# Kernel optimization log

Hardware: AMD Instinct MI355X
Metric: run time of the kernel (lower is better)

The kernel has to match this reference:

```python
import jax, jax.numpy as jnp
import numpy as np

NUM_HEADS = 12
DIM_HEADS = 8  # number of sub-heads the depth is split into


def _split_into_heads(x, num_heads, dim_heads):
    # x: [B, S, E] -> [B, H, D, S, sub]  (D = dim_heads, sub = E/(H*D))
    B, S, E = x.shape
    depth = E // num_heads
    sub = depth // dim_heads
    x = x.reshape(B, S, num_heads, dim_heads, sub)
    return x.transpose(0, 2, 3, 1, 4)  # [B, H, D, S, sub]


def setup_inputs() -> dict:
    key = jax.random.key(0)
    ks = jax.random.split(key, 8)
    B, S, E = 2, 1024, 768
    sc_in = 1.0 / np.sqrt(E)
    return {
        "k": jax.random.normal(ks[0], (B, S, E), dtype=jnp.float32),
        "q": jax.random.normal(ks[1], (B, S, E), dtype=jnp.float32),
        "Wq_w": jax.random.normal(ks[2], (E, E), dtype=jnp.float32) * sc_in,
        "Wq_b": jax.random.normal(ks[3], (E,), dtype=jnp.float32) * 0.01,
        "Wk_w": jax.random.normal(ks[4], (E, E), dtype=jnp.float32) * sc_in,
        "Wk_b": jax.random.normal(ks[5], (E,), dtype=jnp.float32) * 0.01,
        "lin_w": jax.random.normal(ks[6], (DIM_HEADS,), dtype=jnp.float32) * (1.0 / np.sqrt(DIM_HEADS)),
        "lin_b": jax.random.normal(ks[7], (), dtype=jnp.float32) * 0.01,
    }


def reference(k, q, Wq_w, Wq_b, Wk_w, Wk_b, lin_w, lin_b):
    # Linear projections (torch Linear: x @ W^T + b)
    qp = q @ Wq_w.T + Wq_b  # [B, S, E]
    kp = k @ Wk_w.T + Wk_b  # [B, S, E]

    qh = _split_into_heads(qp, NUM_HEADS, DIM_HEADS)  # [B, H, D, S, sub]
    kh = _split_into_heads(kp, NUM_HEADS, DIM_HEADS)  # [B, H, D, S, sub]
    sub = kh.shape[-1]
    scale = 1.0 / np.sqrt(sub).astype(np.float32)

    # Original: scores[b,h,d,i,j] = (qh @ kh^T)/sqrt(sub), permute to [b,h,i,j,d],
    # dropout (identity at eval), then Linear(D,1).squeeze(-1).
    out = jnp.einsum("bhdis,bhdjs,d->bhij", qh, kh, lin_w) * scale + lin_b
    return out  # [B, H, S, S]
```

## Files before the change

kernel.cpp:

```cpp
#include <hip/hip_runtime.h>
#include <hip/hip_bf16.h>

#define S_ 1024
#define E_ 768
#define H_ 12

typedef __bf16  bf16x8 __attribute__((ext_vector_type(8)));
typedef float   f32x4  __attribute__((ext_vector_type(4)));
typedef unsigned short u16x8 __attribute__((ext_vector_type(8)));
typedef unsigned short u16x4 __attribute__((ext_vector_type(4)));

__device__ __forceinline__ unsigned short f2bf(float f) {
    union { float f; unsigned u; } a; a.f = f;
    unsigned u = a.u;
    u += 0x7FFFu + ((u >> 16) & 1u);
    return (unsigned short)(u >> 16);
}

__device__ __forceinline__ u16x8 pack8(float4 a, float4 b) {
    u16x8 o;
    o[0] = f2bf(a.x); o[1] = f2bf(a.y); o[2] = f2bf(a.z); o[3] = f2bf(a.w);
    o[4] = f2bf(b.x); o[5] = f2bf(b.y); o[6] = f2bf(b.z); o[7] = f2bf(b.w);
    return o;
}

__device__ __forceinline__ bf16x8 ld_frag(const char* lbase, int row, int kk, int lane) {
    int cbyte = (kk * 64 + ((lane >> 4) * 16)) ^ ((row & 7) << 4);
    return *(const bf16x8*)(lbase + row * 128 + cbyte);
}

__global__ __launch_bounds__(256) void prep_w_kernel(
    const float* __restrict__ Wq, const float* __restrict__ bq,
    const float* __restrict__ Wk, const float* __restrict__ lin_w,
    unsigned short* __restrict__ Wqbf, unsigned short* __restrict__ Wkbf,
    float* __restrict__ bqs)
{
    const float invs = 0.35355339059327373f;
    int idx4 = blockIdx.x * 256 + threadIdx.x;
    int i = idx4 * 4;
    if (blockIdx.z == 0) {
        int n = i / E_;
        float w = lin_w[(n & 63) >> 3] * invs;
        float4 v = *(const float4*)(Wq + i);
        ushort4 o = make_ushort4(f2bf(v.x * w), f2bf(v.y * w), f2bf(v.z * w), f2bf(v.w * w));
        *(ushort4*)(Wqbf + i) = o;
        if (idx4 < E_) bqs[idx4] = bq[idx4] * (lin_w[(idx4 & 63) >> 3] * invs);
    } else {
        float4 v = *(const float4*)(Wk + i);
        ushort4 o = make_ushort4(f2bf(v.x), f2bf(v.y), f2bf(v.z), f2bf(v.w));
        *(ushort4*)(Wkbf + i) = o;
    }
}

__global__ __launch_bounds__(256) void proj_kernel(
    const float* __restrict__ q_in, const float* __restrict__ k_in,
    const unsigned short* __restrict__ Wqbf, const unsigned short* __restrict__ Wkbf,
    const float* __restrict__ bqs, const float* __restrict__ bk,
    unsigned short* __restrict__ qs, unsigned short* __restrict__ kp)
{
    __shared__ char lds[32768];

    int lid = blockIdx.x;
    int swz = (lid & 7) * 96 + (lid >> 3);
    int z  = swz / 384;
    int rem = swz - z * 384;
    int ty = rem / 12, tx = rem - ty * 12;
    int tm = ty * 64, tn = tx * 64;

    const float* X          = z ? k_in : q_in;
    const unsigned short* W = z ? Wkbf : Wqbf;
    const float* bias       = z ? bk   : bqs;
    unsigned short* P       = z ? kp   : qs;

    int tid = threadIdx.x, lane = tid & 63, wid = tid >> 6;
    int wn = wid >> 1, wm = wid & 1;

    int c0 = tid,        r0 = c0 >> 3, g0 = ((c0 & 7) ^ (r0 & 7)) * 8;
    int c1 = 256 + tid,  r1 = c1 >> 3, g1 = ((c1 & 7) ^ (r1 & 7)) * 8;

    const float* Xg          = X + (size_t)tm * E_;
    const unsigned short* Wg = W + (size_t)tn * E_;

    float4 xv0, xv1, xv2, xv3;
#define LOADX(kb) { \
    const float* xs0 = Xg + r0 * E_ + (kb) + g0; xv0 = *(const float4*)xs0; xv1 = *(const float4*)(xs0 + 4); \
    const float* xs1 = Xg + r1 * E_ + (kb) + g1; xv2 = *(const float4*)xs1; xv3 = *(const float4*)(xs1 + 4); }
#define WRITEX(buf) { \
    char* xb = lds + (buf) * 8192; \
    *(u16x8*)(xb + c0 * 16) = pack8(xv0, xv1); \
    *(u16x8*)(xb + c1 * 16) = pack8(xv2, xv3); }
#define STAGEW(kb, buf) { \
    char* wb = lds + 16384 + (buf) * 8192; \
    __builtin_amdgcn_global_load_lds( \
        (const __attribute__((address_space(1))) void*)(Wg + (size_t)r0 * E_ + (kb) + g0), \
        (__attribute__((address_space(3))) void*)(wb + c0 * 16), 16, 0, 0); \
    __builtin_amdgcn_global_load_lds( \
        (const __attribute__((address_space(1))) void*)(Wg + (size_t)r1 * E_ + (kb) + g1), \
        (__attribute__((address_space(3))) void*)(wb + c1 * 16), 16, 0, 0); }

    f32x4 acc[2][2];
#pragma unroll
    for (int nj = 0; nj < 2; ++nj) {
        int n0 = tn + wn * 32 + nj * 16 + ((lane >> 4) << 2);
        float4 b4 = *(const float4*)(bias + n0);
#pragma unroll
        for (int mi = 0; mi < 2; ++mi)
            acc[nj][mi] = f32x4{b4.x, b4.y, b4.z, b4.w};
    }

#define COMPSTEP(buf) { \
    const char* Xc = lds + (buf) * 8192; \
    const char* Wc = lds + 16384 + (buf) * 8192; \
    _Pragma("unroll") \
    for (int kk = 0; kk < 2; ++kk) { \
        bf16x8 a0 = ld_frag(Wc, wn * 32 + (lane & 15), kk, lane); \
        bf16x8 a1 = ld_frag(Wc, wn * 32 + 16 + (lane & 15), kk, lane); \
        bf16x8 b0 = ld_frag(Xc, wm * 32 + (lane & 15), kk, lane); \
        bf16x8 b1 = ld_frag(Xc, wm * 32 + 16 + (lane & 15), kk, lane); \
        acc[0][0] = __builtin_amdgcn_mfma_f32_16x16x32_bf16(a0, b0, acc[0][0], 0, 0, 0); \
        acc[0][1] = __builtin_amdgcn_mfma_f32_16x16x32_bf16(a0, b1, acc[0][1], 0, 0, 0); \
        acc[1][0] = __builtin_amdgcn_mfma_f32_16x16x32_bf16(a1, b0, acc[1][0], 0, 0, 0); \
        acc[1][1] = __builtin_amdgcn_mfma_f32_16x16x32_bf16(a1, b1, acc[1][1], 0, 0, 0); \
    } }

    STAGEW(0, 0);
    LOADX(0);
    WRITEX(0);
    __syncthreads();
    int cur = 0;
#pragma unroll 2
    for (int t = 0; t < 11; ++t) {
        STAGEW((t + 1) * 64, cur ^ 1);
        LOADX((t + 1) * 64);
        COMPSTEP(cur);
        WRITEX(cur ^ 1);
        __syncthreads();
        cur ^= 1;
    }
    COMPSTEP(cur);

#pragma unroll
    for (int nj = 0; nj < 2; ++nj)
#pragma unroll
        for (int mi = 0; mi < 2; ++mi) {
            int n0 = tn + wn * 32 + nj * 16 + ((lane >> 4) << 2);
            int m  = tm + wm * 32 + mi * 16 + (lane & 15);
            u16x4 pk;
            pk[0] = f2bf(acc[nj][mi][0]); pk[1] = f2bf(acc[nj][mi][1]);
            pk[2] = f2bf(acc[nj][mi][2]); pk[3] = f2bf(acc[nj][mi][3]);
            *(u16x4*)(P + (size_t)m * E_ + n0) = pk;
        }
#undef LOADX
#undef WRITEX
#undef STAGEW
#undef COMPSTEP
}

__global__ __launch_bounds__(256) void scores_kernel(
    const unsigned short* __restrict__ qs, const unsigned short* __restrict__ kp,
    const float* __restrict__ lin_b, float* __restrict__ out)
{
    __shared__ char lds[32768];

    int lid = blockIdx.x;
    int swz = (lid & 7) * 96 + (lid >> 3);
    int z   = swz >> 5;
    int rem = swz & 31;
    int iy  = rem >> 2, jx = rem & 3;
    int b = z / H_, h = z - b * H_;

    int tid = threadIdx.x, lane = tid & 63, wid = tid >> 6;
    int wj = wid >> 1, wi = wid & 1;
    int ti = iy * 128, tj = jx * 256;

    const unsigned short* Qg = qs + (size_t)(b * S_) * E_ + h * 64;
    const unsigned short* Kg = kp + (size_t)(b * S_) * E_ + h * 64;

#define STAGEK(jbase, buf) { \
    char* lb = lds + (buf) * 16384; \
    _Pragma("unroll") \
    for (int pass = 0; pass < 4; ++pass) { \
        int c = pass * 256 + tid; \
        int row = c >> 3, cbg = (c & 7) ^ (row & 7); \
        __builtin_amdgcn_global_load_lds( \
            (const __attribute__((address_space(1))) void*)(Kg + (size_t)((jbase) + row) * E_ + cbg * 8), \
            (__attribute__((address_space(3))) void*)(lb + c * 16), 16, 0, 0); \
    } }

    bf16x8 qf[2][4];
    int qrow = ti + wi * 64 + (lane & 15);
#pragma unroll
    for (int ni = 0; ni < 4; ++ni)
#pragma unroll
        for (int kk = 0; kk < 2; ++kk)
            qf[kk][ni] = *(const bf16x8*)(Qg + (size_t)(qrow + ni * 16) * E_ + kk * 32 + ((lane >> 4) * 8));

    float lb0 = lin_b[0];
    float* O = out + ((size_t)z << 20);

    STAGEK(tj, 0);
    __syncthreads();
    STAGEK(tj + 128, 1);

    f32x4 acc[4][4];

#pragma unroll
    for (int mj = 0; mj < 4; ++mj)
#pragma unroll
        for (int ni = 0; ni < 4; ++ni) acc[mj][ni] = f32x4{lb0, lb0, lb0, lb0};
#pragma unroll
    for (int kk = 0; kk < 2; ++kk) {
        bf16x8 a[4];
#pragma unroll
        for (int mj = 0; mj < 4; ++mj) a[mj] = ld_frag(lds, wj * 64 + mj * 16 + (lane & 15), kk, lane);
#pragma unroll
        for (int mj = 0; mj < 4; ++mj)
#pragma unroll
            for (int ni = 0; ni < 4; ++ni)
                acc[mj][ni] = __builtin_amdgcn_mfma_f32_16x16x32_bf16(a[mj], qf[kk][ni], acc[mj][ni], 0, 0, 0);
    }

    __syncthreads();

#pragma unroll
    for (int mj = 0; mj < 4; ++mj)
#pragma unroll
        for (int ni = 0; ni < 4; ++ni) {
            int i  = ti + wi * 64 + ni * 16 + (lane & 15);
            int j0 = tj + wj * 64 + mj * 16 + ((lane >> 4) << 2);
            *(f32x4*)(O + (size_t)i * S_ + j0) = acc[mj][ni];
        }

#pragma unroll
    for (int mj = 0; mj < 4; ++mj)
#pragma unroll
        for (int ni = 0; ni < 4; ++ni) acc[mj][ni] = f32x4{lb0, lb0, lb0, lb0};
#pragma unroll
    for (int kk = 0; kk < 2; ++kk) {
        bf16x8 a[4];
#pragma unroll
        for (int mj = 0; mj < 4; ++mj) a[mj] = ld_frag(lds + 16384, wj * 64 + mj * 16 + (lane & 15), kk, lane);
#pragma unroll
        for (int mj = 0; mj < 4; ++mj)
#pragma unroll
            for (int ni = 0; ni < 4; ++ni)
                acc[mj][ni] = __builtin_amdgcn_mfma_f32_16x16x32_bf16(a[mj], qf[kk][ni], acc[mj][ni], 0, 0, 0);
    }

#pragma unroll
    for (int mj = 0; mj < 4; ++mj)
#pragma unroll
        for (int ni = 0; ni < 4; ++ni) {
            int i  = ti + wi * 64 + ni * 16 + (lane & 15);
            int j0 = tj + 128 + wj * 64 + mj * 16 + ((lane >> 4) << 2);
            *(f32x4*)(O + (size_t)i * S_ + j0) = acc[mj][ni];
        }
#undef STAGEK
}

extern "C" void kernel_launch(void* const* d_in, const int* in_sizes, int n_in,
                              void* d_out, int out_size, void* d_ws, size_t ws_size,
                              hipStream_t stream)
{
    const float* k_in  = (const float*)d_in[0];
    const float* q_in  = (const float*)d_in[1];
    const float* Wq_w  = (const float*)d_in[2];
    const float* Wq_b  = (const float*)d_in[3];
    const float* Wk_w  = (const float*)d_in[4];
    const float* Wk_b  = (const float*)d_in[5];
    const float* lin_w = (const float*)d_in[6];
    const float* lin_b = (const float*)d_in[7];
    float* out = (float*)d_out;

    char* ws = (char*)d_ws;
    unsigned short* Wqbf = (unsigned short*)(ws + 0);
    unsigned short* Wkbf = (unsigned short*)(ws + 1179648);
    float*          bqs  = (float*)        (ws + 2359296);
    unsigned short* qsb  = (unsigned short*)(ws + 2362368);
    unsigned short* kpb  = (unsigned short*)(ws + 5508096);

    prep_w_kernel<<<dim3(576, 1, 2), dim3(256), 0, stream>>>(Wq_w, Wq_b, Wk_w, lin_w, Wqbf, Wkbf, bqs);
    proj_kernel<<<dim3(768), dim3(256), 0, stream>>>(q_in, k_in, Wqbf, Wkbf, bqs, Wk_b, qsb, kpb);
    scores_kernel<<<dim3(768), dim3(256), 0, stream>>>(qsb, kpb, lin_b, out);
}
```

Before: 45.34 us.

## Pre-cast activations to bf16 and triple-buffer projection with async LDS loads

The fp32-to-bf16 conversion of q and k moves out of the projection GEMM into the prep kernel, which now casts weights and activations in one flat launch. The projection kernel then stages both X and W tiles with global_load_lds into a three-deep LDS ring, using vmcnt waits and raw barriers in place of register loads, packing and __syncthreads. This is meant to hide global latency better and remove conversion ALU work from the GEMM. In exchange, activations take an extra write and read round trip through memory, and LDS per block grows to 48KB, which may lower occupancy.

```diff
diff --git a/kernel.cpp b/kernel.cpp
--- a/kernel.cpp
+++ b/kernel.cpp
@@ -7,7 +7,6 @@
 
 typedef __bf16  bf16x8 __attribute__((ext_vector_type(8)));
 typedef float   f32x4  __attribute__((ext_vector_type(4)));
-typedef unsigned short u16x8 __attribute__((ext_vector_type(8)));
 typedef unsigned short u16x4 __attribute__((ext_vector_type(4)));
 
 __device__ __forceinline__ unsigned short f2bf(float f) {
@@ -17,48 +16,50 @@
     return (unsigned short)(u >> 16);
 }
 
-__device__ __forceinline__ u16x8 pack8(float4 a, float4 b) {
-    u16x8 o;
-    o[0] = f2bf(a.x); o[1] = f2bf(a.y); o[2] = f2bf(a.z); o[3] = f2bf(a.w);
-    o[4] = f2bf(b.x); o[5] = f2bf(b.y); o[6] = f2bf(b.z); o[7] = f2bf(b.w);
-    return o;
-}
-
 __device__ __forceinline__ bf16x8 ld_frag(const char* lbase, int row, int kk, int lane) {
     int cbyte = (kk * 64 + ((lane >> 4) * 16)) ^ ((row & 7) << 4);
     return *(const bf16x8*)(lbase + row * 128 + cbyte);
 }
 
-__global__ __launch_bounds__(256) void prep_w_kernel(
-    const float* __restrict__ Wq, const float* __restrict__ bq,
-    const float* __restrict__ Wk, const float* __restrict__ lin_w,
+__global__ __launch_bounds__(256) void prep_cast_kernel(
+    const float* __restrict__ q_in, const float* __restrict__ k_in,
+    const float* __restrict__ Wq, const float* __restrict__ Wk,
+    const float* __restrict__ bq, const float* __restrict__ lin_w,
     unsigned short* __restrict__ Wqbf, unsigned short* __restrict__ Wkbf,
+    unsigned short* __restrict__ qbf, unsigned short* __restrict__ kbf,
     float* __restrict__ bqs)
 {
     const float invs = 0.35355339059327373f;
-    int idx4 = blockIdx.x * 256 + threadIdx.x;
-    int i = idx4 * 4;
-    if (blockIdx.z == 0) {
+    int u = blockIdx.x * 256 + threadIdx.x;
+    if (u < 147456) {
+        int i = u * 4;
         int n = i / E_;
         float w = lin_w[(n & 63) >> 3] * invs;
         float4 v = *(const float4*)(Wq + i);
-        ushort4 o = make_ushort4(f2bf(v.x * w), f2bf(v.y * w), f2bf(v.z * w), f2bf(v.w * w));
-        *(ushort4*)(Wqbf + i) = o;
-        if (idx4 < E_) bqs[idx4] = bq[idx4] * (lin_w[(idx4 & 63) >> 3] * invs);
+        *(ushort4*)(Wqbf + i) = make_ushort4(f2bf(v.x * w), f2bf(v.y * w), f2bf(v.z * w), f2bf(v.w * w));
+        if (u < E_) bqs[u] = bq[u] * (lin_w[(u & 63) >> 3] * invs);
+    } else if (u < 294912) {
+        int i = (u - 147456) * 4;
+        float4 v = *(const float4*)(Wk + i);
+        *(ushort4*)(Wkbf + i) = make_ushort4(f2bf(v.x), f2bf(v.y), f2bf(v.z), f2bf(v.w));
+    } else if (u < 688128) {
+        int i = (u - 294912) * 4;
+        float4 v = *(const float4*)(q_in + i);
+        *(ushort4*)(qbf + i) = make_ushort4(f2bf(v.x), f2bf(v.y), f2bf(v.z), f2bf(v.w));
     } else {
-        float4 v = *(const float4*)(Wk + i);
-        ushort4 o = make_ushort4(f2bf(v.x), f2bf(v.y), f2bf(v.z), f2bf(v.w));
-        *(ushort4*)(Wkbf + i) = o;
+        int i = (u - 688128) * 4;
+        float4 v = *(const float4*)(k_in + i);
+        *(ushort4*)(kbf + i) = make_ushort4(f2bf(v.x), f2bf(v.y), f2bf(v.z), f2bf(v.w));
     }
 }
 
 __global__ __launch_bounds__(256) void proj_kernel(
-    const float* __restrict__ q_in, const float* __restrict__ k_in,
+    const unsigned short* __restrict__ qbf, const unsigned short* __restrict__ kbf,
     const unsigned short* __restrict__ Wqbf, const unsigned short* __restrict__ Wkbf,
     const float* __restrict__ bqs, const float* __restrict__ bk,
     unsigned short* __restrict__ qs, unsigned short* __restrict__ kp)
 {
-    __shared__ char lds[32768];
+    __shared__ char lds[3 * 16384];
 
     int lid = blockIdx.x;
     int swz = (lid & 7) * 96 + (lid >> 3);
@@ -67,7 +68,7 @@
     int ty = rem / 12, tx = rem - ty * 12;
     int tm = ty * 64, tn = tx * 64;
 
-    const float* X          = z ? k_in : q_in;
+    const unsigned short* X = z ? kbf : qbf;
     const unsigned short* W = z ? Wkbf : Wqbf;
     const float* bias       = z ? bk   : bqs;
     unsigned short* P       = z ? kp   : qs;
@@ -78,25 +79,19 @@
     int c0 = tid,        r0 = c0 >> 3, g0 = ((c0 & 7) ^ (r0 & 7)) * 8;
     int c1 = 256 + tid,  r1 = c1 >> 3, g1 = ((c1 & 7) ^ (r1 & 7)) * 8;
 
-    const float* Xg          = X + (size_t)tm * E_;
+    const unsigned short* Xg = X + (size_t)tm * E_;
     const unsigned short* Wg = W + (size_t)tn * E_;
 
-    float4 xv0, xv1, xv2, xv3;
-#define LOADX(kb) { \
-    const float* xs0 = Xg + r0 * E_ + (kb) + g0; xv0 = *(const float4*)xs0; xv1 = *(const float4*)(xs0 + 4); \
-    const float* xs1 = Xg + r1 * E_ + (kb) + g1; xv2 = *(const float4*)xs1; xv3 = *(const float4*)(xs1 + 4); }
-#define WRITEX(buf) { \
-    char* xb = lds + (buf) * 8192; \
-    *(u16x8*)(xb + c0 * 16) = pack8(xv0, xv1); \
-    *(u16x8*)(xb + c1 * 16) = pack8(xv2, xv3); }
-#define STAGEW(kb, buf) { \
-    char* wb = lds + 16384 + (buf) * 8192; \
-    __builtin_amdgcn_global_load_lds( \
-        (const __attribute__((address_space(1))) void*)(Wg + (size_t)r0 * E_ + (kb) + g0), \
-        (__attribute__((address_space(3))) void*)(wb + c0 * 16), 16, 0, 0); \
-    __builtin_amdgcn_global_load_lds( \
-        (const __attribute__((address_space(1))) void*)(Wg + (size_t)r1 * E_ + (kb) + g1), \
-        (__attribute__((address_space(3))) void*)(wb + c1 * 16), 16, 0, 0); }
+#define GLL(src, dst) __builtin_amdgcn_global_load_lds( \
+        (const __attribute__((address_space(1))) void*)(src), \
+        (__attribute__((address_space(3))) void*)(dst), 16, 0, 0)
+#define STAGE(kb, buf) { \
+    char* xb = lds + (buf) * 16384; \
+    char* wb = xb + 8192; \
+    GLL(Xg + (size_t)r0 * E_ + (kb) + g0, xb + c0 * 16); \
+    GLL(Xg + (size_t)r1 * E_ + (kb) + g1, xb + c1 * 16); \
+    GLL(Wg + (size_t)r0 * E_ + (kb) + g0, wb + c0 * 16); \
+    GLL(Wg + (size_t)r1 * E_ + (kb) + g1, wb + c1 * 16); }
 
     f32x4 acc[2][2];
 #pragma unroll
@@ -109,8 +104,8 @@
     }
 
 #define COMPSTEP(buf) { \
-    const char* Xc = lds + (buf) * 8192; \
-    const char* Wc = lds + 16384 + (buf) * 8192; \
+    const char* Xc = lds + (buf) * 16384; \
+    const char* Wc = Xc + 8192; \
     _Pragma("unroll") \
     for (int kk = 0; kk < 2; ++kk) { \
         bf16x8 a0 = ld_frag(Wc, wn * 32 + (lane & 15), kk, lane); \
@@ -123,20 +118,27 @@
         acc[1][1] = __builtin_amdgcn_mfma_f32_16x16x32_bf16(a1, b1, acc[1][1], 0, 0, 0); \
     } }
 
-    STAGEW(0, 0);
-    LOADX(0);
-    WRITEX(0);
-    __syncthreads();
-    int cur = 0;
-#pragma unroll 2
-    for (int t = 0; t < 11; ++t) {
-        STAGEW((t + 1) * 64, cur ^ 1);
-        LOADX((t + 1) * 64);
+    STAGE(0, 0);
+    STAGE(64, 1);
+
+    int cur = 0, nxt = 2;
+    for (int t = 0; t < 10; ++t) {
+        asm volatile("s_waitcnt vmcnt(4)" ::: "memory");
+        __builtin_amdgcn_s_barrier();
+        __builtin_amdgcn_sched_barrier(0);
+        STAGE((t + 2) * 64, nxt);
         COMPSTEP(cur);
-        WRITEX(cur ^ 1);
-        __syncthreads();
-        cur ^= 1;
-    }
+        cur = cur == 2 ? 0 : cur + 1;
+        nxt = nxt == 2 ? 0 : nxt + 1;
+    }
+    asm volatile("s_waitcnt vmcnt(4)" ::: "memory");
+    __builtin_amdgcn_s_barrier();
+    __builtin_amdgcn_sched_barrier(0);
+    COMPSTEP(cur);
+    cur = cur == 2 ? 0 : cur + 1;
+    asm volatile("s_waitcnt vmcnt(0)" ::: "memory");
+    __builtin_amdgcn_s_barrier();
+    __builtin_amdgcn_sched_barrier(0);
     COMPSTEP(cur);
 
 #pragma unroll
@@ -150,9 +152,8 @@
             pk[2] = f2bf(acc[nj][mi][2]); pk[3] = f2bf(acc[nj][mi][3]);
             *(u16x4*)(P + (size_t)m * E_ + n0) = pk;
         }
-#undef LOADX
-#undef WRITEX
-#undef STAGEW
+#undef GLL
+#undef STAGE
 #undef COMPSTEP
 }
 
@@ -276,10 +277,13 @@
     unsigned short* Wqbf = (unsigned short*)(ws + 0);
     unsigned short* Wkbf = (unsigned short*)(ws + 1179648);
     float*          bqs  = (float*)        (ws + 2359296);
-    unsigned short* qsb  = (unsigned short*)(ws + 2362368);
-    unsigned short* kpb  = (unsigned short*)(ws + 5508096);
-
-    prep_w_kernel<<<dim3(576, 1, 2), dim3(256), 0, stream>>>(Wq_w, Wq_b, Wk_w, lin_w, Wqbf, Wkbf, bqs);
-    proj_kernel<<<dim3(768), dim3(256), 0, stream>>>(q_in, k_in, Wqbf, Wkbf, bqs, Wk_b, qsb, kpb);
+    unsigned short* qbf  = (unsigned short*)(ws + 2362368);
+    unsigned short* kbf  = (unsigned short*)(ws + 5508096);
+    unsigned short* qsb  = (unsigned short*)(ws + 8653824);
+    unsigned short* kpb  = (unsigned short*)(ws + 11799552);
+
+    prep_cast_kernel<<<dim3(4224), dim3(256), 0, stream>>>(q_in, k_in, Wq_w, Wk_w, Wq_b, lin_w,
+                                                           Wqbf, Wkbf, qbf, kbf, bqs);
+    proj_kernel<<<dim3(768), dim3(256), 0, stream>>>(qbf, kbf, Wqbf, Wkbf, bqs, Wk_b, qsb, kpb);
     scores_kernel<<<dim3(768), dim3(256), 0, stream>>>(qsb, kpb, lin_b, out);
 }
```

Result: faster. 42.11 us (-7.1%).
